# Kernel tuning notes

Hardware: AMD Instinct MI355X
Metric: run time of the kernel (lower is better)

The kernel has to match this reference:

```python
import jax, jax.numpy as jnp
import numpy as np

NUM_USERS = 30000
NUM_ITEMS = 70000
N = NUM_USERS + NUM_ITEMS
D = 128
NNZ = 1_000_000
N_LAYERS = 3
BATCH = 16384
EPS = 1e-12  # torch F.normalize default eps
SLOPE = 0.01  # nn.LeakyReLU default negative_slope


def setup_inputs() -> dict:
    key = jax.random.key(0)
    ks = jax.random.split(key, 12)
    return {
        "userIdx": jax.random.randint(ks[0], (BATCH,), 0, NUM_USERS),
        "itemIdx": jax.random.randint(ks[1], (BATCH,), 0, NUM_ITEMS),
        "rows": jax.random.randint(ks[2], (NNZ,), 0, N),
        "cols": jax.random.randint(ks[3], (NNZ,), 0, N),
        "vals": jax.random.uniform(ks[4], (NNZ,), dtype=jnp.float32) * 0.1,
        "uEmbd": jax.random.normal(ks[5], (NUM_USERS, D), dtype=jnp.float32) * 0.1,
        "iEmbd": jax.random.normal(ks[6], (NUM_ITEMS, D), dtype=jnp.float32) * 0.1,
        "Wlin": jax.random.normal(ks[7], (N_LAYERS, D, D), dtype=jnp.float32) / np.sqrt(D),
        "blin": jax.random.normal(ks[8], (N_LAYERS, D), dtype=jnp.float32) * 0.01,
        "Wint": jax.random.normal(ks[9], (N_LAYERS, D, D), dtype=jnp.float32) / np.sqrt(D),
        "bint": jax.random.normal(ks[10], (N_LAYERS, D), dtype=jnp.float32) * 0.01,
    }


def reference(userIdx, itemIdx, rows, cols, vals, uEmbd, iEmbd, Wlin, blin, Wint, bint):
    num_users = uEmbd.shape[0]
    n = uEmbd.shape[0] + iEmbd.shape[0]
    features = jnp.concatenate([uEmbd, iEmbd], axis=0)  # [N, D]
    embds = [features]
    for l in range(Wlin.shape[0]):
        # SpMM: L @ features via gather + segment_sum over COO edges
        Lx = jax.ops.segment_sum(vals[:, None] * features[cols], rows, num_segments=n)
        # (L + I) @ f then linear
        part1 = (Lx + features) @ Wlin[l] + blin[l]
        # (L @ f) * f then linear
        part2 = (Lx * features) @ Wint[l] + bint[l]
        features = jax.nn.leaky_relu(part1 + part2, negative_slope=SLOPE)
        norm = jnp.maximum(jnp.linalg.norm(features, axis=1, keepdims=True), EPS)
        features = features / norm
        embds.append(features)
    finalEmbd = jnp.concatenate(embds, axis=1)  # [N, D*(1+n_layers)]
    u = finalEmbd[userIdx]
    i = finalEmbd[itemIdx + num_users]
    return jnp.sum(u * i, axis=1)
```

## Files before the change

### kernel.cpp

```cpp
#include <hip/hip_runtime.h>
#include <hip/hip_bf16.h>

#define NU 30000
#define NI 70000
#define NN 100000
#define DD 128
#define NLAYERS 3
#define SLOPE_ 0.01f
#define EPS_ 1e-12f

#define NB 782
#define NBKT 1024
#define NBLK 256
#define AROW 136
#define MAXL 32768
#define BM 64

typedef __bf16 v8bf __attribute__((ext_vector_type(8)));
typedef float v16f __attribute__((ext_vector_type(16)));
typedef float v2f __attribute__((ext_vector_type(2)));
typedef unsigned short ushort_t;

union UB8 { uint4 u; v8bf v; };

__device__ __forceinline__ float bflo(unsigned u) { return __uint_as_float(u << 16); }
__device__ __forceinline__ float bfhi(unsigned u) { return __uint_as_float(u & 0xffff0000u); }

__device__ __forceinline__ unsigned pk2(float a, float b) {
    __hip_bfloat162 h = __float22bfloat162_rn(make_float2(a, b));
    return *reinterpret_cast<unsigned*>(&h);
}
__device__ __forceinline__ uint4 pk8(const float* f) {
    return make_uint4(pk2(f[0], f[1]), pk2(f[2], f[3]), pk2(f[4], f[5]), pk2(f[6], f[7]));
}
__device__ __forceinline__ void unp8(uint4 g, float* f) {
    f[0] = bflo(g.x); f[1] = bfhi(g.x);
    f[2] = bflo(g.y); f[3] = bfhi(g.y);
    f[4] = bflo(g.z); f[5] = bfhi(g.z);
    f[6] = bflo(g.w); f[7] = bfhi(g.w);
}
__device__ __forceinline__ ushort_t f2bf1(float x) {
    __hip_bfloat16 h = __float2bfloat16(x);
    return *reinterpret_cast<ushort_t*>(&h);
}

__global__ __launch_bounds__(256) void k_concat_bf(const float* __restrict__ u,
                                                   const float* __restrict__ it,
                                                   ushort_t* __restrict__ fb) {
    int idx = blockIdx.x * 256 + threadIdx.x;
    if (idx >= NN * DD / 8) return;
    size_t base = (size_t)idx * 8;
    const float* src = (base < (size_t)NU * DD) ? (u + base) : (it + base - (size_t)NU * DD);
    float f[8];
    float4 a = *(const float4*)src;
    float4 b = *(const float4*)(src + 4);
    f[0] = a.x; f[1] = a.y; f[2] = a.z; f[3] = a.w;
    f[4] = b.x; f[5] = b.y; f[6] = b.z; f[7] = b.w;
    *(uint4*)(fb + base) = pk8(f);
}

__device__ __forceinline__ void dot_wave(const ushort_t* __restrict__ fb,
                                         const int* __restrict__ uIdx,
                                         const int* __restrict__ iIdx,
                                         float* __restrict__ out,
                                         int batch, int accum, int b, int lane) {
    if (b >= batch) return;
    unsigned ua = *(const unsigned*)(fb + (size_t)uIdx[b] * DD + lane * 2);
    unsigned ib = *(const unsigned*)(fb + (size_t)(iIdx[b] + NU) * DD + lane * 2);
    float s = bflo(ua) * bflo(ib) + bfhi(ua) * bfhi(ib);
#pragma unroll
    for (int m = 32; m; m >>= 1) s += __shfl_xor(s, m, 64);
    if (lane == 0) out[b] = accum ? out[b] + s : s;
}

__global__ __launch_bounds__(256) void k_dot(const ushort_t* __restrict__ fb,
                                             const int* __restrict__ uIdx,
                                             const int* __restrict__ iIdx,
                                             float* __restrict__ out,
                                             int batch, int accum) {
    dot_wave(fb, uIdx, iIdx, out, batch, accum,
             blockIdx.x * 4 + (threadIdx.x >> 6), threadIdx.x & 63);
}

__global__ __launch_bounds__(1024) void k_lhist(const int* __restrict__ rows,
                                                int* __restrict__ ghist,
                                                int* __restrict__ flags,
                                                int nnz, int epb) {
    __shared__ int h[NBKT];
    int t = threadIdx.x, b = blockIdx.x;
    h[t] = 0;
    int i0 = b * 1024 + t;
    if (i0 < NN) flags[i0] = 0;
    __syncthreads();
    int e0 = b * epb, e1 = min(e0 + epb, nnz);
    for (int e = e0 + t; e < e1; e += 1024) atomicAdd(&h[rows[e] >> 7], 1);
    __syncthreads();
    ghist[t * NBLK + b] = h[t];
}

__global__ __launch_bounds__(256) void k_rscan(int* __restrict__ ghist,
                                               int* __restrict__ btot,
                                               const int* __restrict__ uIdx,
                                               const int* __restrict__ iIdx,
                                               int* __restrict__ flags,
                                               int* __restrict__ cnt, int batch) {
    int t = threadIdx.x;
    int gid = blockIdx.x * 256 + t;
    if (gid == 0) *cnt = 0;
    if (gid < batch) flags[uIdx[gid]] = 1;
    else if (gid < 2 * batch) flags[iIdx[gid - batch] + NU] = 1;

    int bkt = blockIdx.x * 4 + (t >> 6);
    int lane = t & 63;
    int* row = ghist + bkt * NBLK;
    int4 c = *(const int4*)(row + lane * 4);
    int s = c.x + c.y + c.z + c.w;
    int incl = s;
#pragma unroll
    for (int m = 1; m < 64; m <<= 1) {
        int o = __shfl_up(incl, m, 64);
        if (lane >= m) incl += o;
    }
    int excl = incl - s;
    int4 o;
    o.x = excl;
    o.y = o.x + c.x;
    o.z = o.y + c.y;
    o.w = o.z + c.z;
    *(int4*)(row + lane * 4) = o;
    if (lane == 63) btot[bkt] = incl;
}

__global__ __launch_bounds__(256) void k_btscan(const int* __restrict__ btot,
                                                int* __restrict__ bbase) {
    int t = threadIdx.x;
    int4 c = *(const int4*)(btot + t * 4);
    int tsum = c.x + c.y + c.z + c.w;
    int incl = tsum;
#pragma unroll
    for (int m = 1; m < 64; m <<= 1) {
        int o = __shfl_up(incl, m, 64);
        if ((t & 63) >= m) incl += o;
    }
    __shared__ int wsum[4];
    if ((t & 63) == 63) wsum[t >> 6] = incl;
    __syncthreads();
    int off = 0;
    for (int i = 0; i < (t >> 6); ++i) off += wsum[i];
    int excl = off + incl - tsum;
    int4 o;
    o.x = excl;
    o.y = o.x + c.x;
    o.z = o.y + c.y;
    o.w = o.z + c.z;
    *(int4*)(bbase + t * 4) = o;
    if (t == 255) bbase[NBKT] = o.w + c.w;
}

__global__ __launch_bounds__(1024) void k_sscatter(const int* __restrict__ rows,
                                                   const int* __restrict__ cols,
                                                   const float* __restrict__ vals,
                                                   const int* __restrict__ ghist,
                                                   const int* __restrict__ bbase,
                                                   int2* __restrict__ bedges,
                                                   const int* __restrict__ flags,
                                                   int* __restrict__ list,
                                                   int* __restrict__ cnt,
                                                   int nnz, int epb) {
    __shared__ int base[NBKT];
    __shared__ int h[NBKT];
    int t = threadIdx.x, b = blockIdx.x;
    base[t] = bbase[t] + ghist[t * NBLK + b];
    h[t] = 0;
    int lane = t & 63;
    int i = b * 1024 + t;
    int f = (i < NN) ? flags[i] : 0;
    unsigned long long mask = __ballot(f);
    int total = __popcll(mask);
    int prefix = __popcll(mask & ((1ULL << lane) - 1));
    int bs = 0;
    if (lane == 0 && total) bs = atomicAdd(cnt, total);
    bs = __shfl(bs, 0, 64);
    if (f) list[bs + prefix] = i;
    __syncthreads();
    int e0 = b * epb, e1 = min(e0 + epb, nnz);
    for (int e = e0 + t; e < e1; e += 1024) {
        int r = rows[e];
        int bkt = r >> 7;
        int rank = atomicAdd(&h[bkt], 1);
        bedges[base[bkt] + rank] = make_int2(((r & 127) << 20) | cols[e],
                                             __float_as_int(vals[e]));
    }
}

__global__ __launch_bounds__(256) void k_csort(const int* __restrict__ bbase,
                                               const int2* __restrict__ bedges,
                                               int2* __restrict__ edges,
                                               int* __restrict__ rowPtr, int nnz) {
    __shared__ int cntS[128];
    __shared__ int fillS[128];
    __shared__ int wtot;
    int b = blockIdx.x, t = threadIdx.x;
    int s0 = bbase[b];
    int s1 = bbase[b + 1];
    if (t < 128) cntS[t] = 0;
    __syncthreads();
    for (int i = s0 + t; i < s1; i += 256) atomicAdd(&cntS[bedges[i].x >> 20], 1);
    __syncthreads();
    int v = 0, incl = 0;
    if (t < 128) {
        v = cntS[t];
        incl = v;
#pragma unroll
        for (int m = 1; m < 64; m <<= 1) {
            int o = __shfl_up(incl, m, 64);
            if ((t & 63) >= m) incl += o;
        }
        if (t == 63) wtot = incl;
    }
    __syncthreads();
    if (t < 128) {
        int excl = incl - v + ((t >= 64) ? wtot : 0);
        fillS[t] = excl;
        int gr = b * 128 + t;
        if (gr < NN) rowPtr[gr] = s0 + excl;
    }
    if (b == 0 && t == 0) rowPtr[NN] = nnz;
    __syncthreads();
    for (int i = s0 + t; i < s1; i += 256) {
        int2 e = bedges[i];
        int r = e.x >> 20;
        int p = atomicAdd(&fillS[r], 1);
        edges[s0 + p] = make_int2(e.x & 0xFFFFF, e.y);
    }
}

__global__ __launch_bounds__(256) void k_wprep(const float* __restrict__ Wlin,
                                               const float* __restrict__ Wint,
                                               uint4* __restrict__ Wb4) {
    int id = blockIdx.x * 256 + threadIdx.x;
    int lane = id & 63;
    int w = (id >> 6) & 3;
    int s = (id >> 8) & 7;
    int c = (id >> 11) & 1;
    int l = id >> 12;
    const float* src = (c ? Wint : Wlin) + (size_t)l * DD * DD;
    int n = w * 32 + (lane & 31);
    int k0 = s * 16 + ((lane >> 5) & 1) * 8;
    float f[8];
#pragma unroll
    for (int j = 0; j < 8; ++j) f[j] = src[(size_t)(k0 + j) * DD + n];
    Wb4[id] = pk8(f);
}

__device__ __forceinline__ void acc_pk(v2f* acc2, uint4 g, float v) {
    v2f vv = {v, v};
    unsigned gw[4] = {g.x, g.y, g.z, g.w};
#pragma unroll
    for (int p = 0; p < 4; ++p) {
        v2f x = {bflo(gw[p]), bfhi(gw[p])};
        acc2[p] = x * vv + acc2[p];
    }
}

template <bool INDEXED>
__device__ __forceinline__ void flayer_body(int bid,
                                            const int* __restrict__ rowPtr,
                                            const int2* __restrict__ edges,
                                            const uint4* __restrict__ Wb4,
                                            const float* __restrict__ blin,
                                            const float* __restrict__ bint,
                                            const ushort_t* __restrict__ fin,
                                            ushort_t* __restrict__ fout,
                                            const int* __restrict__ list, int nc) {
    __shared__ ushort_t As[2][BM * AROW];
    __shared__ float pnormAll[BM * 4];
    __shared__ float rinvS[BM];
    __shared__ int rowIdS[BM];

    const int t = threadIdx.x;
    const int w = t >> 6;
    const int l = t & 63;
    const int mt = w >> 2;
    const int w2 = w & 3;
    const int q = l >> 5;
    const int ln = l & 31;
    const int n = w2 * 32 + ln;
    const int m0 = bid * BM;

    if (INDEXED && m0 >= nc) return;

    if (t < BM) {
        int gi = m0 + t;
        int gm;
        if (INDEXED) gm = (gi < nc) ? list[gi] : -1;
        else gm = (gi < NN) ? gi : -1;
        rowIdS[t] = gm;
    }
    __syncthreads();

    {
        const int qi = t >> 4;
        const int d0 = (t & 15) * 8;
#pragma unroll
        for (int j = 0; j < 2; ++j) {
            int row = qi * 2 + j;
            int gm = rowIdS[row];
            uint4 sv = make_uint4(0, 0, 0, 0);
            uint4 pv = make_uint4(0, 0, 0, 0);
            if (gm >= 0) {
                int beg = rowPtr[gm], end = rowPtr[gm + 1];
                v2f acc2[4];
#pragma unroll
                for (int p = 0; p < 4; ++p) acc2[p] = (v2f){0.f, 0.f};
                int e = beg;
                for (; e + 3 < end; e += 4) {
                    int2 p0 = edges[e];
                    int2 p1 = edges[e + 1];
                    int2 p2 = edges[e + 2];
                    int2 p3 = edges[e + 3];
                    uint4 g0 = *(const uint4*)(fin + (size_t)p0.x * DD + d0);
                    uint4 g1 = *(const uint4*)(fin + (size_t)p1.x * DD + d0);
                    uint4 g2 = *(const uint4*)(fin + (size_t)p2.x * DD + d0);
                    uint4 g3 = *(const uint4*)(fin + (size_t)p3.x * DD + d0);
                    acc_pk(acc2, g0, __int_as_float(p0.y));
                    acc_pk(acc2, g1, __int_as_float(p1.y));
                    acc_pk(acc2, g2, __int_as_float(p2.y));
                    acc_pk(acc2, g3, __int_as_float(p3.y));
                }
                if (e + 1 < end) {
                    int2 p0 = edges[e];
                    int2 p1 = edges[e + 1];
                    uint4 g0 = *(const uint4*)(fin + (size_t)p0.x * DD + d0);
                    uint4 g1 = *(const uint4*)(fin + (size_t)p1.x * DD + d0);
                    acc_pk(acc2, g0, __int_as_float(p0.y));
                    acc_pk(acc2, g1, __int_as_float(p1.y));
                    e += 2;
                }
                if (e < end) {
                    int2 p0 = edges[e];
                    uint4 g0 = *(const uint4*)(fin + (size_t)p0.x * DD + d0);
                    acc_pk(acc2, g0, __int_as_float(p0.y));
                }
                float a[8], b8[8], r8[8];
#pragma unroll
                for (int p = 0; p < 4; ++p) {
                    a[2 * p] = acc2[p][0];
                    a[2 * p + 1] = acc2[p][1];
                }
                uint4 gf = *(const uint4*)(fin + (size_t)gm * DD + d0);
                unp8(gf, b8);
#pragma unroll
                for (int k = 0; k < 8; ++k) r8[k] = a[k] + b8[k];
                sv = pk8(r8);
#pragma unroll
                for (int k = 0; k < 8; ++k) r8[k] = a[k] * b8[k];
                pv = pk8(r8);
            }
            *(uint4*)&As[0][row * AROW + d0] = sv;
            *(uint4*)&As[1][row * AROW + d0] = pv;
        }
    }
    __syncthreads();

    const float bias = blin[n] + bint[n];
    v16f acc;
#pragma unroll
    for (int i = 0; i < 16; ++i) acc[i] = 0.f;

#pragma unroll
    for (int c = 0; c < 2; ++c) {
#pragma unroll
        for (int sh = 0; sh < 2; ++sh) {
            UB8 bf[4];
#pragma unroll
            for (int k = 0; k < 4; ++k)
                bf[k].u = Wb4[c * 2048 + (sh * 4 + k) * 256 + w2 * 64 + l];
#pragma unroll
            for (int k = 0; k < 4; ++k) {
                v8bf af = *(const v8bf*)&As[c][(mt * 32 + ln) * AROW + (sh * 4 + k) * 16 + q * 8];
                acc = __builtin_amdgcn_mfma_f32_32x32x16_bf16(af, bf[k].v, acc, 0, 0, 0);
            }
        }
    }

    float r[16];
#pragma unroll
    for (int reg = 0; reg < 16; ++reg) {
        float v = acc[reg] + bias;
        v = (v > 0.f) ? v : SLOPE_ * v;
        acc[reg] = v;
        r[reg] = v * v;
    }
#pragma unroll
    for (int lev = 0; lev < 4; ++lev) {
        int m = 1 << lev;
        int cnt2 = 8 >> lev;
        bool hi = (l & m) != 0;
#pragma unroll
        for (int i = 0; i < 8; ++i) {
            if (i < cnt2) {
                float p = hi ? r[2 * i + 1] : r[2 * i];
                float qv = hi ? r[2 * i] : r[2 * i + 1];
                r[i] = p + __shfl_xor(qv, m, 64);
            }
        }
    }
    float tot = r[0] + __shfl_xor(r[0], 16, 64);
    if ((l & 31) < 16) {
        int i = l & 15;
        int row = (i & 3) + ((i >> 2) << 3) + 4 * q;
        pnormAll[(mt * 32 + row) * 4 + w2] = tot;
    }
    __syncthreads();
    if (t < BM) {
        float4 p = *(const float4*)&pnormAll[t * 4];
        float s = p.x + p.y + p.z + p.w;
        rinvS[t] = 1.0f / fmaxf(sqrtf(s), EPS_);
    }
    __syncthreads();

#pragma unroll
    for (int reg = 0; reg < 16; ++reg) {
        int row = (reg & 3) + ((reg >> 2) << 3) + 4 * q;
        int gm = rowIdS[mt * 32 + row];
        if (gm >= 0)
            fout[(size_t)gm * DD + n] = f2bf1(acc[reg] * rinvS[mt * 32 + row]);
    }
}

__global__ __launch_bounds__(512, 8) void k_flayer(const int* __restrict__ rowPtr,
                                                   const int2* __restrict__ edges,
                                                   const uint4* __restrict__ Wb4,
                                                   const float* __restrict__ blin,
                                                   const float* __restrict__ bint,
                                                   const ushort_t* __restrict__ fin,
                                                   ushort_t* __restrict__ fout,
                                                   const int* __restrict__ uIdx,
                                                   const int* __restrict__ iIdx,
                                                   float* __restrict__ out,
                                                   int batch, int accum, int dotBlocks) {
    if ((int)blockIdx.x < dotBlocks) {
        dot_wave(fin, uIdx, iIdx, out, batch, accum,
                 blockIdx.x * 8 + (threadIdx.x >> 6), threadIdx.x & 63);
        return;
    }
    flayer_body<false>(blockIdx.x - dotBlocks, rowPtr, edges, Wb4, blin, bint,
                       fin, fout, nullptr, 0);
}

__global__ __launch_bounds__(512, 8) void k_flayer_idx(const int* __restrict__ rowPtr,
                                                       const int2* __restrict__ edges,
                                                       const uint4* __restrict__ Wb4,
                                                       const float* __restrict__ blin,
                                                       const float* __restrict__ bint,
                                                       const ushort_t* __restrict__ fin,
                                                       ushort_t* __restrict__ fout,
                                                       const int* __restrict__ list,
                                                       const int* __restrict__ cnt,
                                                       const int* __restrict__ uIdx,
                                                       const int* __restrict__ iIdx,
                                                       float* __restrict__ out,
                                                       int batch, int dotBlocks) {
    if ((int)blockIdx.x < dotBlocks) {
        dot_wave(fin, uIdx, iIdx, out, batch, 1,
                 blockIdx.x * 8 + (threadIdx.x >> 6), threadIdx.x & 63);
        return;
    }
    flayer_body<true>(blockIdx.x - dotBlocks, rowPtr, edges, Wb4, blin, bint,
                      fin, fout, list, *cnt);
}

extern "C" void kernel_launch(void* const* d_in, const int* in_sizes, int n_in,
                              void* d_out, int out_size, void* d_ws, size_t ws_size,
                              hipStream_t stream) {
    const int*   userIdx = (const int*)d_in[0];
    const int*   itemIdx = (const int*)d_in[1];
    const int*   rows    = (const int*)d_in[2];
    const int*   cols    = (const int*)d_in[3];
    const float* vals    = (const float*)d_in[4];
    const float* uE      = (const float*)d_in[5];
    const float* iE      = (const float*)d_in[6];
    const float* Wlin    = (const float*)d_in[7];
    const float* blin    = (const float*)d_in[8];
    const float* Wint    = (const float*)d_in[9];
    const float* bint    = (const float*)d_in[10];
    float* out = (float*)d_out;

    const int batch = in_sizes[0];
    const int nnz   = in_sizes[2];
    const int epb   = (nnz + NBLK - 1) / NBLK;
    const int dotB8 = (batch + 7) / 8;
    const int dotB4 = (batch + 3) / 4;

    ushort_t* featA = (ushort_t*)d_ws;
    ushort_t* featB = featA + (size_t)NN * DD;
    uint4* Wb4      = (uint4*)(featB + (size_t)NN * DD);
    int2*  bedges   = (int2*)(Wb4 + 12288);
    int2*  edges    = bedges + nnz;
    int*   ghist    = (int*)(edges + nnz);
    int*   btot     = ghist + NBKT * NBLK;
    int*   bbase    = btot + NBKT;
    int*   rowPtr   = bbase + NBKT + 4;
    int*   flags    = rowPtr + NN + 4;
    int*   list     = flags + NN;
    int*   cnt      = list + MAXL;

    k_concat_bf<<<(NN * DD / 8 + 255) / 256, 256, 0, stream>>>(uE, iE, featA);
    k_wprep<<<48, 256, 0, stream>>>(Wlin, Wint, Wb4);

    k_lhist<<<NBLK, 1024, 0, stream>>>(rows, ghist, flags, nnz, epb);
    k_rscan<<<NBKT / 4, 256, 0, stream>>>(ghist, btot, userIdx, itemIdx, flags, cnt, batch);
    k_btscan<<<1, 256, 0, stream>>>(btot, bbase);
    k_sscatter<<<NBLK, 1024, 0, stream>>>(rows, cols, vals, ghist, bbase, bedges,
                                          flags, list, cnt, nnz, epb);
    k_csort<<<NB, 256, 0, stream>>>(bbase, bedges, edges, rowPtr, nnz);

    k_flayer<<<dotB8 + (NN + BM - 1) / BM, 512, 0, stream>>>(
        rowPtr, edges, Wb4, blin, bint, featA, featB,
        userIdx, itemIdx, out, batch, 0, dotB8);

    k_flayer<<<dotB8 + (NN + BM - 1) / BM, 512, 0, stream>>>(
        rowPtr, edges, Wb4 + 4096, blin + DD, bint + DD, featB, featA,
        userIdx, itemIdx, out, batch, 1, dotB8);

    k_flayer_idx<<<dotB8 + (MAXL + BM - 1) / BM, 512, 0, stream>>>(
        rowPtr, edges, Wb4 + 8192, blin + 2 * DD, bint + 2 * DD, featA, featB,
        list, cnt, userIdx, itemIdx, out, batch, dotB8);

    k_dot<<<dotB4, 256, 0, stream>>>(featB, userIdx, itemIdx, out, batch, 1);
}
```

Baseline: 314.1 us.

## Balance SpMM edges across threads with merge-path split and LDS atomics

For the non-indexed layer path, the block's whole edge range is split evenly across 32 row-groups of threads instead of assigning each thread pair of rows. Partial sums are flushed into an fp32 shared-memory tile with atomicAdd whenever a row boundary is crossed, and the tile aliases the A-operand buffer. This targets load imbalance from skewed row degrees, at the cost of LDS atomics, extra barriers and a separate pass to build the sum/product tiles.

New measurement: 464.4 us. +47.8%, slower.

```diff
diff --git a/kernel.cpp b/kernel.cpp
--- a/kernel.cpp
+++ b/kernel.cpp
@@ -263,6 +263,15 @@
     }
 }
 
+__device__ __forceinline__ void flushq(float* fx, int cur, int d0, v2f* acc2) {
+#pragma unroll
+    for (int p = 0; p < 4; ++p) {
+        atomicAdd(&fx[cur * DD + d0 + 2 * p], acc2[p][0]);
+        atomicAdd(&fx[cur * DD + d0 + 2 * p + 1], acc2[p][1]);
+        acc2[p] = (v2f){0.f, 0.f};
+    }
+}
+
 template <bool INDEXED>
 __device__ __forceinline__ void flayer_body(int bid,
                                             const int* __restrict__ rowPtr,
@@ -273,10 +282,15 @@
                                             const ushort_t* __restrict__ fin,
                                             ushort_t* __restrict__ fout,
                                             const int* __restrict__ list, int nc) {
-    __shared__ ushort_t As[2][BM * AROW];
+    __shared__ uint4 tileRaw[2176];
     __shared__ float pnormAll[BM * 4];
     __shared__ float rinvS[BM];
     __shared__ int rowIdS[BM];
+    __shared__ int rpS[BM + 1];
+
+    ushort_t* As0 = (ushort_t*)tileRaw;
+    ushort_t* As1 = As0 + BM * AROW;
+    float* fx = (float*)tileRaw;
 
     const int t = threadIdx.x;
     const int w = t >> 6;
@@ -297,9 +311,13 @@
         else gm = (gi < NN) ? gi : -1;
         rowIdS[t] = gm;
     }
-    __syncthreads();
-
-    {
+    if (!INDEXED && t >= BM && t <= 2 * BM) {
+        int gi = m0 + (t - BM);
+        rpS[t - BM] = rowPtr[min(gi, NN)];
+    }
+    __syncthreads();
+
+    if (INDEXED) {
         const int qi = t >> 4;
         const int d0 = (t & 15) * 8;
 #pragma unroll
@@ -357,11 +375,99 @@
                 for (int k = 0; k < 8; ++k) r8[k] = a[k] * b8[k];
                 pv = pk8(r8);
             }
-            *(uint4*)&As[0][row * AROW + d0] = sv;
-            *(uint4*)&As[1][row * AROW + d0] = pv;
-        }
-    }
-    __syncthreads();
+            *(uint4*)&As0[row * AROW + d0] = sv;
+            *(uint4*)&As1[row * AROW + d0] = pv;
+        }
+        __syncthreads();
+    } else {
+        {
+            uint4 z = make_uint4(0, 0, 0, 0);
+#pragma unroll
+            for (int i = 0; i < 4; ++i) tileRaw[i * 512 + t] = z;
+        }
+        __syncthreads();
+        const int beg = rpS[0], end = rpS[BM];
+        const int nE = end - beg;
+        if (nE > 0) {
+            const int qi = t >> 4;
+            const int d0 = (t & 15) * 8;
+            const int epq = (nE + 31) >> 5;
+            const int qBeg = beg + qi * epq;
+            const int qEnd = min(qBeg + epq, end);
+            if (qBeg < qEnd) {
+                int cur = 0;
+#pragma unroll
+                for (int s = 32; s; s >>= 1) {
+                    int nx = cur + s;
+                    if (nx < BM && rpS[nx] <= qBeg) cur = nx;
+                }
+                int nextB = rpS[cur + 1];
+                v2f acc2[4];
+#pragma unroll
+                for (int p = 0; p < 4; ++p) acc2[p] = (v2f){0.f, 0.f};
+                int e = qBeg;
+                while (e < qEnd) {
+                    int n4 = qEnd - e;
+                    if (n4 > 4) n4 = 4;
+                    int2 p[4];
+                    uint4 g[4];
+#pragma unroll
+                    for (int j = 0; j < 4; ++j)
+                        if (j < n4) p[j] = edges[e + j];
+#pragma unroll
+                    for (int j = 0; j < 4; ++j)
+                        if (j < n4) g[j] = *(const uint4*)(fin + (size_t)p[j].x * DD + d0);
+#pragma unroll
+                    for (int j = 0; j < 4; ++j) {
+                        if (j < n4) {
+                            while (e + j >= nextB) {
+                                flushq(fx, cur, d0, acc2);
+                                ++cur;
+                                nextB = rpS[cur + 1];
+                            }
+                            acc_pk(acc2, g[j], __int_as_float(p[j].y));
+                        }
+                    }
+                    e += n4;
+                }
+                flushq(fx, cur, d0, acc2);
+            }
+        }
+        __syncthreads();
+        uint4 svr[2], pvr[2];
+#pragma unroll
+        for (int ii = 0; ii < 2; ++ii) {
+            int idx = ii * 512 + t;
+            int row = idx >> 4;
+            int ch = idx & 15;
+            int gm = rowIdS[row];
+            svr[ii] = make_uint4(0, 0, 0, 0);
+            pvr[ii] = make_uint4(0, 0, 0, 0);
+            if (gm >= 0) {
+                float a[8], b8[8], r8[8];
+#pragma unroll
+                for (int k = 0; k < 8; ++k) a[k] = fx[row * DD + ch * 8 + k];
+                uint4 gf = *(const uint4*)(fin + (size_t)gm * DD + ch * 8);
+                unp8(gf, b8);
+#pragma unroll
+                for (int k = 0; k < 8; ++k) r8[k] = a[k] + b8[k];
+                svr[ii] = pk8(r8);
+#pragma unroll
+                for (int k = 0; k < 8; ++k) r8[k] = a[k] * b8[k];
+                pvr[ii] = pk8(r8);
+            }
+        }
+        __syncthreads();
+#pragma unroll
+        for (int ii = 0; ii < 2; ++ii) {
+            int idx = ii * 512 + t;
+            int row = idx >> 4;
+            int ch = idx & 15;
+            *(uint4*)&As0[row * AROW + ch * 8] = svr[ii];
+            *(uint4*)&As1[row * AROW + ch * 8] = pvr[ii];
+        }
+        __syncthreads();
+    }
 
     const float bias = blin[n] + bint[n];
     v16f acc;
@@ -370,6 +476,7 @@
 
 #pragma unroll
     for (int c = 0; c < 2; ++c) {
+        const ushort_t* Asc = c ? As1 : As0;
 #pragma unroll
         for (int sh = 0; sh < 2; ++sh) {
             UB8 bf[4];
@@ -378,7 +485,7 @@
                 bf[k].u = Wb4[c * 2048 + (sh * 4 + k) * 256 + w2 * 64 + l];
 #pragma unroll
             for (int k = 0; k < 4; ++k) {
-                v8bf af = *(const v8bf*)&As[c][(mt * 32 + ln) * AROW + (sh * 4 + k) * 16 + q * 8];
+                v8bf af = *(const v8bf*)&Asc[(mt * 32 + ln) * AROW + (sh * 4 + k) * 16 + q * 8];
                 acc = __builtin_amdgcn_mfma_f32_32x32x16_bf16(af, bf[k].v, acc, 0, 0, 0);
             }
         }
```

## Fuse CSR build, concat and weight prep into one cooperative kernel

Applied to the files above, without the earlier changes.

Replaces seven preprocessing launches (bf16 concat, weight repack, histogram, row scan, bucket scan, scatter, per-bucket sort) with a single cooperative kernel of 256 blocks that uses grid-wide syncs between phases. The aim is to remove per-launch overhead and inter-kernel gaps on the setup path. In exchange, phases that used many small blocks (concat, csort over 782 buckets) now run on only 256 blocks of 1024 threads with grid-stride loops, and grid.sync adds its own cost.

New measurement: 468.0 us. +49.0%, slower.

```diff
diff --git a/kernel.cpp b/kernel.cpp
--- a/kernel.cpp
+++ b/kernel.cpp
@@ -1,5 +1,8 @@
 #include <hip/hip_runtime.h>
 #include <hip/hip_bf16.h>
+#include <hip/hip_cooperative_groups.h>
+
+namespace cg = cooperative_groups;
 
 #define NU 30000
 #define NI 70000
@@ -42,21 +45,6 @@
 __device__ __forceinline__ ushort_t f2bf1(float x) {
     __hip_bfloat16 h = __float2bfloat16(x);
     return *reinterpret_cast<ushort_t*>(&h);
-}
-
-__global__ __launch_bounds__(256) void k_concat_bf(const float* __restrict__ u,
-                                                   const float* __restrict__ it,
-                                                   ushort_t* __restrict__ fb) {
-    int idx = blockIdx.x * 256 + threadIdx.x;
-    if (idx >= NN * DD / 8) return;
-    size_t base = (size_t)idx * 8;
-    const float* src = (base < (size_t)NU * DD) ? (u + base) : (it + base - (size_t)NU * DD);
-    float f[8];
-    float4 a = *(const float4*)src;
-    float4 b = *(const float4*)(src + 4);
-    f[0] = a.x; f[1] = a.y; f[2] = a.z; f[3] = a.w;
-    f[4] = b.x; f[5] = b.y; f[6] = b.z; f[7] = b.w;
-    *(uint4*)(fb + base) = pk8(f);
 }
 
 __device__ __forceinline__ void dot_wave(const ushort_t* __restrict__ fb,
@@ -82,175 +70,180 @@
              blockIdx.x * 4 + (threadIdx.x >> 6), threadIdx.x & 63);
 }
 
-__global__ __launch_bounds__(1024) void k_lhist(const int* __restrict__ rows,
-                                                int* __restrict__ ghist,
-                                                int* __restrict__ flags,
-                                                int nnz, int epb) {
-    __shared__ int h[NBKT];
-    int t = threadIdx.x, b = blockIdx.x;
-    h[t] = 0;
-    int i0 = b * 1024 + t;
-    if (i0 < NN) flags[i0] = 0;
+__global__ __launch_bounds__(1024, 4) void k_build(
+    const int* __restrict__ rows, const int* __restrict__ cols,
+    const float* __restrict__ vals,
+    const float* __restrict__ uE, const float* __restrict__ iE,
+    const float* __restrict__ Wlin, const float* __restrict__ Wint,
+    ushort_t* __restrict__ fb, uint4* __restrict__ Wb4,
+    int* __restrict__ ghist, int* __restrict__ btot, int* __restrict__ bbase,
+    int* __restrict__ rowPtr, int* __restrict__ flags,
+    int* __restrict__ list, int* __restrict__ cnt,
+    int2* __restrict__ bedges, int2* __restrict__ edges,
+    const int* __restrict__ uIdx, const int* __restrict__ iIdx,
+    int batch, int nnz, int epb) {
+    cg::grid_group grid = cg::this_grid();
+    __shared__ int sh[2048];
+    const int t = threadIdx.x;
+    const int b = blockIdx.x;
+    const int gtid = b * 1024 + t;
+
+    for (int idx = gtid; idx < NN * DD / 8; idx += NBLK * 1024) {
+        size_t base = (size_t)idx * 8;
+        const float* src = (base < (size_t)NU * DD) ? (uE + base)
+                                                    : (iE + base - (size_t)NU * DD);
+        float f[8];
+        float4 a = *(const float4*)src;
+        float4 b4 = *(const float4*)(src + 4);
+        f[0] = a.x; f[1] = a.y; f[2] = a.z; f[3] = a.w;
+        f[4] = b4.x; f[5] = b4.y; f[6] = b4.z; f[7] = b4.w;
+        *(uint4*)(fb + base) = pk8(f);
+    }
+    if (gtid < 12288) {
+        int id = gtid;
+        int lane = id & 63;
+        int w = (id >> 6) & 3;
+        int s = (id >> 8) & 7;
+        int c = (id >> 11) & 1;
+        int l = id >> 12;
+        const float* src = (c ? Wint : Wlin) + (size_t)l * DD * DD;
+        int n = w * 32 + (lane & 31);
+        int k0 = s * 16 + ((lane >> 5) & 1) * 8;
+        float f[8];
+#pragma unroll
+        for (int j = 0; j < 8; ++j) f[j] = src[(size_t)(k0 + j) * DD + n];
+        Wb4[id] = pk8(f);
+    }
+    sh[t] = 0;
+    sh[1024 + t] = 0;
+    if (gtid < NN) flags[gtid] = 0;
     __syncthreads();
-    int e0 = b * epb, e1 = min(e0 + epb, nnz);
-    for (int e = e0 + t; e < e1; e += 1024) atomicAdd(&h[rows[e] >> 7], 1);
+    {
+        int e0 = b * epb, e1 = min(e0 + epb, nnz);
+        for (int e = e0 + t; e < e1; e += 1024) atomicAdd(&sh[rows[e] >> 7], 1);
+    }
     __syncthreads();
-    ghist[t * NBLK + b] = h[t];
-}
-
-__global__ __launch_bounds__(256) void k_rscan(int* __restrict__ ghist,
-                                               int* __restrict__ btot,
-                                               const int* __restrict__ uIdx,
-                                               const int* __restrict__ iIdx,
-                                               int* __restrict__ flags,
-                                               int* __restrict__ cnt, int batch) {
-    int t = threadIdx.x;
-    int gid = blockIdx.x * 256 + t;
-    if (gid == 0) *cnt = 0;
-    if (gid < batch) flags[uIdx[gid]] = 1;
-    else if (gid < 2 * batch) flags[iIdx[gid - batch] + NU] = 1;
-
-    int bkt = blockIdx.x * 4 + (t >> 6);
-    int lane = t & 63;
-    int* row = ghist + bkt * NBLK;
-    int4 c = *(const int4*)(row + lane * 4);
-    int s = c.x + c.y + c.z + c.w;
-    int incl = s;
-#pragma unroll
-    for (int m = 1; m < 64; m <<= 1) {
-        int o = __shfl_up(incl, m, 64);
-        if (lane >= m) incl += o;
-    }
-    int excl = incl - s;
-    int4 o;
-    o.x = excl;
-    o.y = o.x + c.x;
-    o.z = o.y + c.y;
-    o.w = o.z + c.z;
-    *(int4*)(row + lane * 4) = o;
-    if (lane == 63) btot[bkt] = incl;
-}
-
-__global__ __launch_bounds__(256) void k_btscan(const int* __restrict__ btot,
-                                                int* __restrict__ bbase) {
-    int t = threadIdx.x;
-    int4 c = *(const int4*)(btot + t * 4);
-    int tsum = c.x + c.y + c.z + c.w;
-    int incl = tsum;
-#pragma unroll
-    for (int m = 1; m < 64; m <<= 1) {
-        int o = __shfl_up(incl, m, 64);
-        if ((t & 63) >= m) incl += o;
-    }
-    __shared__ int wsum[4];
-    if ((t & 63) == 63) wsum[t >> 6] = incl;
-    __syncthreads();
-    int off = 0;
-    for (int i = 0; i < (t >> 6); ++i) off += wsum[i];
-    int excl = off + incl - tsum;
-    int4 o;
-    o.x = excl;
-    o.y = o.x + c.x;
-    o.z = o.y + c.y;
-    o.w = o.z + c.z;
-    *(int4*)(bbase + t * 4) = o;
-    if (t == 255) bbase[NBKT] = o.w + c.w;
-}
-
-__global__ __launch_bounds__(1024) void k_sscatter(const int* __restrict__ rows,
-                                                   const int* __restrict__ cols,
-                                                   const float* __restrict__ vals,
-                                                   const int* __restrict__ ghist,
-                                                   const int* __restrict__ bbase,
-                                                   int2* __restrict__ bedges,
-                                                   const int* __restrict__ flags,
-                                                   int* __restrict__ list,
-                                                   int* __restrict__ cnt,
-                                                   int nnz, int epb) {
-    __shared__ int base[NBKT];
-    __shared__ int h[NBKT];
-    int t = threadIdx.x, b = blockIdx.x;
-    base[t] = bbase[t] + ghist[t * NBLK + b];
-    h[t] = 0;
-    int lane = t & 63;
-    int i = b * 1024 + t;
-    int f = (i < NN) ? flags[i] : 0;
-    unsigned long long mask = __ballot(f);
-    int total = __popcll(mask);
-    int prefix = __popcll(mask & ((1ULL << lane) - 1));
-    int bs = 0;
-    if (lane == 0 && total) bs = atomicAdd(cnt, total);
-    bs = __shfl(bs, 0, 64);
-    if (f) list[bs + prefix] = i;
-    __syncthreads();
-    int e0 = b * epb, e1 = min(e0 + epb, nnz);
-    for (int e = e0 + t; e < e1; e += 1024) {
-        int r = rows[e];
-        int bkt = r >> 7;
-        int rank = atomicAdd(&h[bkt], 1);
-        bedges[base[bkt] + rank] = make_int2(((r & 127) << 20) | cols[e],
-                                             __float_as_int(vals[e]));
-    }
-}
-
-__global__ __launch_bounds__(256) void k_csort(const int* __restrict__ bbase,
-                                               const int2* __restrict__ bedges,
-                                               int2* __restrict__ edges,
-                                               int* __restrict__ rowPtr, int nnz) {
-    __shared__ int cntS[128];
-    __shared__ int fillS[128];
-    __shared__ int wtot;
-    int b = blockIdx.x, t = threadIdx.x;
-    int s0 = bbase[b];
-    int s1 = bbase[b + 1];
-    if (t < 128) cntS[t] = 0;
-    __syncthreads();
-    for (int i = s0 + t; i < s1; i += 256) atomicAdd(&cntS[bedges[i].x >> 20], 1);
-    __syncthreads();
-    int v = 0, incl = 0;
-    if (t < 128) {
-        v = cntS[t];
-        incl = v;
+    ghist[t * NBLK + b] = sh[t];
+    grid.sync();
+
+    if (gtid == 0) *cnt = 0;
+    if (gtid < batch) flags[uIdx[gtid]] = 1;
+    else if (gtid < 2 * batch) flags[iIdx[gtid - batch] + NU] = 1;
+    {
+        int wg = gtid >> 6;
+        if (wg < NBKT) {
+            int lane = t & 63;
+            int* rowp = ghist + wg * NBLK;
+            int4 c = *(const int4*)(rowp + lane * 4);
+            int s = c.x + c.y + c.z + c.w;
+            int incl = s;
+#pragma unroll
+            for (int m = 1; m < 64; m <<= 1) {
+                int o = __shfl_up(incl, m, 64);
+                if (lane >= m) incl += o;
+            }
+            int excl = incl - s;
+            int4 o;
+            o.x = excl;
+            o.y = o.x + c.x;
+            o.z = o.y + c.y;
+            o.w = o.z + c.z;
+            *(int4*)(rowp + lane * 4) = o;
+            if (lane == 63) btot[wg] = incl;
+        }
+    }
+    grid.sync();
+
+    if (b == 0) {
+        int4 c = make_int4(0, 0, 0, 0);
+        if (t < 256) c = *(const int4*)(btot + t * 4);
+        int tsum = c.x + c.y + c.z + c.w;
+        int incl = tsum;
 #pragma unroll
         for (int m = 1; m < 64; m <<= 1) {
             int o = __shfl_up(incl, m, 64);
             if ((t & 63) >= m) incl += o;
         }
-        if (t == 63) wtot = incl;
-    }
-    __syncthreads();
-    if (t < 128) {
-        int excl = incl - v + ((t >= 64) ? wtot : 0);
-        fillS[t] = excl;
-        int gr = b * 128 + t;
-        if (gr < NN) rowPtr[gr] = s0 + excl;
-    }
-    if (b == 0 && t == 0) rowPtr[NN] = nnz;
-    __syncthreads();
-    for (int i = s0 + t; i < s1; i += 256) {
-        int2 e = bedges[i];
-        int r = e.x >> 20;
-        int p = atomicAdd(&fillS[r], 1);
-        edges[s0 + p] = make_int2(e.x & 0xFFFFF, e.y);
-    }
-}
-
-__global__ __launch_bounds__(256) void k_wprep(const float* __restrict__ Wlin,
-                                               const float* __restrict__ Wint,
-                                               uint4* __restrict__ Wb4) {
-    int id = blockIdx.x * 256 + threadIdx.x;
-    int lane = id & 63;
-    int w = (id >> 6) & 3;
-    int s = (id >> 8) & 7;
-    int c = (id >> 11) & 1;
-    int l = id >> 12;
-    const float* src = (c ? Wint : Wlin) + (size_t)l * DD * DD;
-    int n = w * 32 + (lane & 31);
-    int k0 = s * 16 + ((lane >> 5) & 1) * 8;
-    float f[8];
-#pragma unroll
-    for (int j = 0; j < 8; ++j) f[j] = src[(size_t)(k0 + j) * DD + n];
-    Wb4[id] = pk8(f);
+        if (t < 256 && (t & 63) == 63) sh[t >> 6] = incl;
+        __syncthreads();
+        if (t < 256) {
+            int off = 0;
+            for (int i = 0; i < (t >> 6); ++i) off += sh[i];
+            int excl = off + incl - tsum;
+            int4 o;
+            o.x = excl;
+            o.y = o.x + c.x;
+            o.z = o.y + c.y;
+            o.w = o.z + c.z;
+            *(int4*)(bbase + t * 4) = o;
+            if (t == 255) bbase[NBKT] = o.w + c.w;
+        }
+    }
+    grid.sync();
+
+    {
+        int* base = sh;
+        int* h2 = sh + 1024;
+        base[t] = bbase[t] + ghist[t * NBLK + b];
+        h2[t] = 0;
+        int lane = t & 63;
+        int f = (gtid < NN) ? flags[gtid] : 0;
+        unsigned long long mask = __ballot(f);
+        int total = __popcll(mask);
+        int prefix = __popcll(mask & ((1ULL << lane) - 1));
+        int bs = 0;
+        if (lane == 0 && total) bs = atomicAdd(cnt, total);
+        bs = __shfl(bs, 0, 64);
+        if (f) list[bs + prefix] = gtid;
+        __syncthreads();
+        int e0 = b * epb, e1 = min(e0 + epb, nnz);
+        for (int e = e0 + t; e < e1; e += 1024) {
+            int r = rows[e];
+            int bkt = r >> 7;
+            int rank = atomicAdd(&h2[bkt], 1);
+            bedges[base[bkt] + rank] = make_int2(((r & 127) << 20) | cols[e],
+                                                 __float_as_int(vals[e]));
+        }
+    }
+    grid.sync();
+
+    for (int bk = b; bk < NB; bk += NBLK) {
+        int s0 = bbase[bk];
+        int s1 = bbase[bk + 1];
+        int* cntS = sh;
+        int* fillS = sh + 128;
+        if (t < 128) cntS[t] = 0;
+        __syncthreads();
+        for (int i = s0 + t; i < s1; i += 1024) atomicAdd(&cntS[bedges[i].x >> 20], 1);
+        __syncthreads();
+        int v = 0, incl = 0;
+        if (t < 128) {
+            v = cntS[t];
+            incl = v;
+#pragma unroll
+            for (int m = 1; m < 64; m <<= 1) {
+                int o = __shfl_up(incl, m, 64);
+                if ((t & 63) >= m) incl += o;
+            }
+            if (t == 63) sh[256] = incl;
+        }
+        __syncthreads();
+        if (t < 128) {
+            int excl = incl - v + ((t >= 64) ? sh[256] : 0);
+            fillS[t] = excl;
+            int gr = bk * 128 + t;
+            if (gr < NN) rowPtr[gr] = s0 + excl;
+        }
+        if (bk == 0 && t == 0) rowPtr[NN] = nnz;
+        __syncthreads();
+        for (int i = s0 + t; i < s1; i += 1024) {
+            int2 e = bedges[i];
+            int r = e.x >> 20;
+            int p = atomicAdd(&fillS[r], 1);
+            edges[s0 + p] = make_int2(e.x & 0xFFFFF, e.y);
+        }
+        __syncthreads();
+    }
 }
 
 __device__ __forceinline__ void acc_pk(v2f* acc2, uint4 g, float v) {
@@ -487,9 +480,9 @@
     const float* bint    = (const float*)d_in[10];
     float* out = (float*)d_out;
 
-    const int batch = in_sizes[0];
-    const int nnz   = in_sizes[2];
-    const int epb   = (nnz + NBLK - 1) / NBLK;
+    int batch = in_sizes[0];
+    int nnz   = in_sizes[2];
+    int epb   = (nnz + NBLK - 1) / NBLK;
     const int dotB8 = (batch + 7) / 8;
     const int dotB4 = (batch + 3) / 4;
 
@@ -506,15 +499,15 @@
     int*   list     = flags + NN;
     int*   cnt      = list + MAXL;
 
-    k_concat_bf<<<(NN * DD / 8 + 255) / 256, 256, 0, stream>>>(uE, iE, featA);
-    k_wprep<<<48, 256, 0, stream>>>(Wlin, Wint, Wb4);
-
-    k_lhist<<<NBLK, 1024, 0, stream>>>(rows, ghist, flags, nnz, epb);
-    k_rscan<<<NBKT / 4, 256, 0, stream>>>(ghist, btot, userIdx, itemIdx, flags, cnt, batch);
-    k_btscan<<<1, 256, 0, stream>>>(btot, bbase);
-    k_sscatter<<<NBLK, 1024, 0, stream>>>(rows, cols, vals, ghist, bbase, bedges,
-                                          flags, list, cnt, nnz, epb);
-    k_csort<<<NB, 256, 0, stream>>>(bbase, bedges, edges, rowPtr, nnz);
+    void* args[] = {(void*)&rows,  (void*)&cols,  (void*)&vals,
+                    (void*)&uE,    (void*)&iE,    (void*)&Wlin, (void*)&Wint,
+                    (void*)&featA, (void*)&Wb4,
+                    (void*)&ghist, (void*)&btot,  (void*)&bbase,
+                    (void*)&rowPtr,(void*)&flags, (void*)&list, (void*)&cnt,
+                    (void*)&bedges,(void*)&edges,
+                    (void*)&userIdx,(void*)&itemIdx,
+                    (void*)&batch, (void*)&nnz,   (void*)&epb};
+    hipLaunchCooperativeKernel((void*)k_build, dim3(NBLK), dim3(1024), args, 0, stream);
 
     k_flayer<<<dotB8 + (NN + BM - 1) / BM, 512, 0, stream>>>(
         rowPtr, edges, Wb4, blin, bint, featA, featB,
```
